# Kernel tuning notes

Hardware: AMD Instinct MI355X
Metric: run time of the kernel (lower is better)

The kernel has to match this reference:

```python
import jax, jax.numpy as jnp
import numpy as np

N = 50000   # num_entities
F = 300     # node feature dim
D = 128     # embedding_dim
H = 4       # heads
C = D // H  # per-head out channels (32)
E = 640000  # num edges
R = 200     # num_relations
L = 2       # num_layers
NEG_SLOPE = 0.2  # PyG GATv2Conv default


def setup_inputs() -> dict:
    key = jax.random.key(0)
    ks = jax.random.split(key, 14)
    s = 0.1
    return {
        "entity": jnp.arange(N, dtype=jnp.int32),
        "edge_index": jax.random.randint(ks[0], (2, E), 0, N, dtype=jnp.int32),
        "edge_type": jax.random.randint(ks[1], (E,), 0, R, dtype=jnp.int32),
        # learned parameters
        "node_features": jax.random.normal(ks[2], (N, F), jnp.float32) * s,   # entity_embedding table
        "rel_emb": jax.random.normal(ks[3], (R, D), jnp.float32) * s,          # relation_embedding
        "proj_w": jax.random.normal(ks[4], (F, D), jnp.float32) * s,           # project Linear
        "proj_b": jnp.zeros((D,), jnp.float32),
        # per-layer GATv2Conv params, stacked over L layers
        "w_l": jax.random.normal(ks[5], (L, D, H * C), jnp.float32) * s,       # lin_l weight
        "b_l": jnp.zeros((L, H * C), jnp.float32),
        "w_r": jax.random.normal(ks[6], (L, D, H * C), jnp.float32) * s,       # lin_r weight
        "b_r": jnp.zeros((L, H * C), jnp.float32),
        "w_e": jax.random.normal(ks[7], (L, D, H * C), jnp.float32) * s,       # lin_edge weight (no bias)
        "att": jax.random.normal(ks[8], (L, H, C), jnp.float32) * s,           # attention vector a
        "bias": jnp.zeros((L, H * C), jnp.float32),                             # output bias
    }


def _gatv2_layer(x, src, dst, edge_attr, w_l, b_l, w_r, b_r, w_e, att, bias):
    # x: [N, D], edge_attr: [E, D]
    x_l = (x @ w_l + b_l).reshape(N, H, C)
    x_r = (x @ w_r + b_r).reshape(N, H, C)
    e = (edge_attr @ w_e).reshape(E, H, C)
    # per-edge message (gather src/dst + edge), GATv2: leaky_relu BEFORE attention dot
    m = jax.nn.leaky_relu(x_l[src] + x_r[dst] + e, NEG_SLOPE)   # [E, H, C]
    logits = jnp.einsum('ehc,hc->eh', m, att)                    # [E, H]
    # segment softmax over edges grouped by destination node
    lmax = jax.ops.segment_max(logits, dst, num_segments=N)      # [N, H]
    ex = jnp.exp(logits - lmax[dst])                             # [E, H]
    denom = jax.ops.segment_sum(ex, dst, num_segments=N)         # [N, H]
    alpha = ex / denom[dst]                                      # [E, H]
    # scatter-aggregate messages x_l[src] weighted by alpha
    out = jax.ops.segment_sum(x_l[src] * alpha[:, :, None], dst, num_segments=N)  # [N, H, C]
    return out.reshape(N, H * C) + bias


def reference(entity, edge_index, edge_type, node_features, rel_emb,
              proj_w, proj_b, w_l, b_l, w_r, b_r, w_e, att, bias):
    x = node_features[entity]            # embedding lookup
    x = x @ proj_w + proj_b              # project to D
    edge_attr = rel_emb[edge_type]       # [E, D] (weights=False -> no edge_weight scaling)
    src, dst = edge_index[0], edge_index[1]
    for i in range(L):
        x = _gatv2_layer(x, src, dst, edge_attr,
                         w_l[i], b_l[i], w_r[i], b_r[i], w_e[i], att[i], bias[i])
        if i != L - 1:
            x = jax.nn.elu(x)            # dropout inactive (eval mode)
    return x
```

## Files before the change

kernel.cpp:

```cpp
#include <hip/hip_runtime.h>

#define NN 50000
#define FF 300
#define DD 128
#define HH 4
#define CC 32
#define EE 640000
#define RR 200
#define LL 2
#define SB ((NN + 255) / 256)
#define PK 320
#define WCONV (2 * 128 * 128)
#define WTOT (2 * 128 * PK + WCONV)
#define HB ((EE + 255) / 256)
#define WB (WCONV / 256)
#define FB PK
#define RB (LL * RR / 2)

typedef unsigned short u16;
typedef unsigned int u32;
typedef _Float16 h2   __attribute__((ext_vector_type(2)));
typedef _Float16 half8 __attribute__((ext_vector_type(8)));
typedef __attribute__((ext_vector_type(4))) float floatx4;

__device__ __forceinline__ u16 f2h(float f) {
    union { _Float16 h; u16 u; } v; v.h = (_Float16)f; return v.u;
}
__device__ __forceinline__ float h2f(u16 u) {
    union { u16 u; _Float16 h; } v; v.u = u; return (float)v.h;
}
__device__ __forceinline__ h2 u2h2(u32 p) {
    union { u32 u; h2 h; } v; v.u = p; return v.h;
}
__device__ __forceinline__ h2 hmax2(h2 a, h2 b) {
#if __has_builtin(__builtin_elementwise_max)
    return __builtin_elementwise_max(a, b);
#else
    h2 r; r.x = a.x > b.x ? a.x : b.x; r.y = a.y > b.y ? a.y : b.y; return r;
#endif
}
__device__ __forceinline__ float hdot2(h2 a, h2 b, float c) {
#if __has_builtin(__builtin_amdgcn_fdot2)
    return __builtin_amdgcn_fdot2(a, b, c, false);
#else
    return c + (float)a.x * (float)b.x + (float)a.y * (float)b.y;
#endif
}

__device__ __forceinline__ int block_excl_scan(int v, int* lds4, int* total) {
    int lane = threadIdx.x & 63, wid = threadIdx.x >> 6;
    int x = v;
    #pragma unroll
    for (int off = 1; off < 64; off <<= 1) {
        int y = __shfl_up(x, off, 64);
        if (lane >= off) x += y;
    }
    if (lane == 63) lds4[wid] = x;
    __syncthreads();
    int add = 0;
    #pragma unroll
    for (int w = 0; w < 4; w++) add += (w < wid) ? lds4[w] : 0;
    *total = lds4[0] + lds4[1] + lds4[2] + lds4[3];
    return x + add - v;
}

__global__ __launch_bounds__(256)
void prep_kernel(const int* __restrict__ ei, int* __restrict__ counts,
                 const float* __restrict__ proj_w, const float* __restrict__ w_l,
                 const float* __restrict__ w_r, u16* __restrict__ wt,
                 const float* __restrict__ rel_emb, const float* __restrict__ w_e,
                 u16* __restrict__ erel, const float* __restrict__ proj_b,
                 const float* __restrict__ b_l, const float* __restrict__ b_r,
                 float* __restrict__ fbias)
{
    __shared__ float rv[2][DD];
    int b = blockIdx.x, tid = threadIdx.x;
    if (b < HB) {
        int e = b * 256 + tid;
        if (e < EE) atomicAdd(&counts[ei[EE + e]], 1);
    } else if (b < HB + WB) {
        int i = (b - HB) * 256 + tid;
        int seg = i >> 14;
        int r = i & 16383;
        int n = r >> 7, k = r & 127;
        const float* src = (seg == 0 ? w_l : w_r) + (size_t)DD * DD;
        wt[2 * 128 * PK + i] = f2h(src[(size_t)k * DD + n]);
    } else if (b < HB + WB + FB) {
        int half = tid >> 7, d = tid & 127;
        int pp = (b - HB - WB) * 2 + half;
        int lr = pp / PK, k = pp - lr * PK;
        rv[half][d] = (k < FF) ? proj_w[(size_t)k * DD + d] : 0.f;
        __syncthreads();
        float acc = 0.f;
        if (k < FF) {
            const float* W = lr ? w_r : w_l;
            #pragma unroll 8
            for (int j = 0; j < DD; j++) acc += rv[half][j] * W[(size_t)j * DD + d];
        }
        wt[(size_t)lr * 128 * PK + (size_t)d * PK + k] = f2h(acc);
    } else if (b == HB + WB + FB) {
        int half = tid >> 7, d = tid & 127;
        if (tid < DD) rv[0][tid] = proj_b[tid];
        __syncthreads();
        const float* W = half ? w_r : w_l;
        float acc = half ? b_r[d] : b_l[d];
        #pragma unroll 8
        for (int j = 0; j < DD; j++) acc += rv[0][j] * W[(size_t)j * DD + d];
        fbias[half * DD + d] = acc;
    } else {
        int half = tid >> 7, d = tid & 127;
        int lr = (b - HB - WB - FB - 1) * 2 + half;
        int l = lr / RR, r = lr - l * RR;
        rv[half][d] = rel_emb[r * DD + d];
        __syncthreads();
        const float* W = w_e + (size_t)l * DD * DD;
        float acc = 0.f;
        #pragma unroll 8
        for (int k = 0; k < DD; k++) acc += rv[half][k] * W[k * DD + d];
        erel[(size_t)lr * DD + d] = f2h(acc);
    }
}

template<bool AF16, bool GATHER>
__global__ __launch_bounds__(256)
void gemm_dual_kernel(const void* __restrict__ A_, const int* __restrict__ rowidx,
                      int lda, int K, int Ka, int ldb,
                      const u16* __restrict__ BT1, const float* __restrict__ bias1,
                      u16* __restrict__ C1,
                      const u16* __restrict__ BT2, const float* __restrict__ bias2,
                      u16* __restrict__ C2, int M)
{
    __shared__ u16 As[64][72];
    __shared__ u16 Bs[256][72];
    int tid  = threadIdx.x;
    int m0   = blockIdx.x * 64;
    int wave = tid >> 6, lane = tid & 63;
    int quad = lane >> 4, l16 = lane & 15;
    int wcol = wave * 64;

    floatx4 acc[4][4];
    #pragma unroll
    for (int i = 0; i < 4; i++)
        #pragma unroll
        for (int j = 0; j < 4; j++) acc[i][j] = (floatx4){0.f, 0.f, 0.f, 0.f};

    int ar = tid >> 2, ak = (tid & 3) * 16;
    int arow = m0 + ar;
    int rid = (arow < M) ? (GATHER ? rowidx[arow] : arow) : 0;
    const u16* Brow = (tid < 128) ? (BT1 + (size_t)tid * ldb)
                                  : (BT2 + (size_t)(tid - 128) * ldb);

    for (int kk = 0; kk < K; kk += 64) {
        int kb = kk + ak;
        u16 tmp[16];
        if (AF16) {
            const u16* Ap = (const u16*)A_ + (size_t)rid * lda + kb;
            if (kb + 16 <= Ka) {
                *(half8*)&tmp[0] = *(const half8*)Ap;
                *(half8*)&tmp[8] = *(const half8*)(Ap + 8);
            } else {
                #pragma unroll
                for (int j = 0; j < 16; j++) tmp[j] = (kb + j < Ka) ? Ap[j] : (u16)0;
            }
        } else {
            const float* Ap = (const float*)A_ + (size_t)rid * lda + kb;
            if (kb + 16 <= Ka) {
                #pragma unroll
                for (int qq = 0; qq < 4; qq++) {
                    float4 f = *(const float4*)(Ap + qq * 4);
                    tmp[qq*4+0] = f2h(f.x); tmp[qq*4+1] = f2h(f.y);
                    tmp[qq*4+2] = f2h(f.z); tmp[qq*4+3] = f2h(f.w);
                }
            } else {
                #pragma unroll
                for (int j = 0; j < 16; j++) tmp[j] = (kb + j < Ka) ? f2h(Ap[j]) : (u16)0;
            }
        }
        *(half8*)&As[ar][ak]     = *(half8*)&tmp[0];
        *(half8*)&As[ar][ak + 8] = *(half8*)&tmp[8];
        #pragma unroll
        for (int q = 0; q < 8; q++)
            *(half8*)&Bs[tid][q * 8] = *(const half8*)(Brow + kk + q * 8);
        __syncthreads();
        #pragma unroll
        for (int ks = 0; ks < 2; ks++) {
            half8 af[4], bf[4];
            #pragma unroll
            for (int i = 0; i < 4; i++)
                af[i] = *(const half8*)&As[i * 16 + l16][ks * 32 + quad * 8];
            #pragma unroll
            for (int j = 0; j < 4; j++)
                bf[j] = *(const half8*)&Bs[wcol + j * 16 + l16][ks * 32 + quad * 8];
            #pragma unroll
            for (int i = 0; i < 4; i++)
                #pragma unroll
                for (int j = 0; j < 4; j++)
                    acc[i][j] = __builtin_amdgcn_mfma_f32_16x16x32_f16(
                        af[i], bf[j], acc[i][j], 0, 0, 0);
        }
        __syncthreads();
    }

    u16* Cw = (wave < 2) ? C1 : C2;
    const float* bw = (wave < 2) ? bias1 : bias2;
    int cbase = wcol & 127;
    #pragma unroll
    for (int i = 0; i < 4; i++) {
        #pragma unroll
        for (int rr = 0; rr < 4; rr++) {
            int row = m0 + i * 16 + quad * 4 + rr;
            if (row < M) {
                #pragma unroll
                for (int j = 0; j < 4; j++) {
                    int col = cbase + j * 16 + l16;
                    Cw[(size_t)row * DD + col] = f2h(acc[i][j][rr] + bw[col]);
                }
            }
        }
    }
}

__global__ __launch_bounds__(256)
void scan_local_kernel(const int* __restrict__ counts, int* __restrict__ offsets,
                       int* __restrict__ bsum)
{
    __shared__ int lds4[4];
    int i = blockIdx.x * 256 + threadIdx.x;
    int v = (i < NN) ? counts[i] : 0;
    int total;
    int ex = block_excl_scan(v, lds4, &total);
    if (i < NN) offsets[i] = ex;
    if (threadIdx.x == 0) bsum[blockIdx.x] = total;
}

__global__ __launch_bounds__(256)
void scan_bsum_kernel(int* __restrict__ bsum)
{
    __shared__ int lds4[4];
    int t = threadIdx.x;
    int v = (t < SB) ? bsum[t] : 0;
    int total;
    int ex = block_excl_scan(v, lds4, &total);
    if (t < SB) bsum[t] = ex;
}

__global__ __launch_bounds__(256)
void scatter_kernel(const int* __restrict__ ei, const int* __restrict__ et,
                    const int* __restrict__ offsets, const int* __restrict__ bsum,
                    int* __restrict__ fill, u32* __restrict__ dstorder)
{
    int e = blockIdx.x * 256 + threadIdx.x;
    if (e >= EE) return;
    int d = ei[EE + e];
    int pos = offsets[d] + bsum[d >> 8] + atomicAdd(&fill[d], 1);
    dstorder[pos] = (u32)ei[e] | ((u32)et[e] << 16);
}

__global__ __launch_bounds__(256)
void node_kernel(const u32* __restrict__ dstorder, const int* __restrict__ offsets,
                 const int* __restrict__ bsum,
                 const u16* __restrict__ xl, const u16* __restrict__ xr,
                 const u16* __restrict__ erel, const float* __restrict__ att,
                 const float* __restrict__ bias,
                 u16* __restrict__ xnext, float* __restrict__ outp, int is_last)
{
    int tid  = threadIdx.x;
    int node = blockIdx.x * 4 + (tid >> 6);
    int lane = tid & 63;
    if (node >= NN) return;
    int g  = lane >> 3;
    int gl = lane & 7;
    int c0 = gl * 16;
    int beg = offsets[node] + bsum[node >> 8];
    int end = (node == NN - 1) ? EE : offsets[node + 1] + bsum[(node + 1) >> 8];

    h2 xrh[8], atth[8];
    {
        const u32* xp = (const u32*)&xr[(size_t)node * DD + c0];
        #pragma unroll
        for (int q = 0; q < 8; q++) xrh[q] = u2h2(xp[q]);
        #pragma unroll
        for (int q = 0; q < 8; q++) {
            float2 av = *(const float2*)&att[c0 + q * 2];
            atth[q] = (h2){(_Float16)av.x, (_Float16)av.y};
        }
    }
    const h2 c02 = (h2){(_Float16)0.2f, (_Float16)0.2f};

    float s = 0.f;
    h2 a2[8];
    #pragma unroll
    for (int q = 0; q < 8; q++) a2[q] = (h2){(_Float16)0.f, (_Float16)0.f};

    int es = beg + g;
    u32 stB = (es + 8 < end) ? dstorder[es + 8] : 0u;
    h2 xhA[8], ehA[8];
    {
        u32 stA = (es < end) ? dstorder[es] : 0u;
        int src = stA & 0xffff, typ = stA >> 16;
        const u32* xp = (const u32*)&xl[(size_t)src * DD + c0];
        const u32* ep = (const u32*)&erel[(size_t)typ * DD + c0];
        #pragma unroll
        for (int q = 0; q < 8; q++) { xhA[q] = u2h2(xp[q]); ehA[q] = u2h2(ep[q]); }
    }

    for (int base = beg; base < end; base += 8) {
        u32 stN = (base + 16 + g < end) ? dstorder[base + 16 + g] : 0u;
        h2 xhB[8], ehB[8];
        {
            int src = stB & 0xffff, typ = stB >> 16;
            const u32* xp = (const u32*)&xl[(size_t)src * DD + c0];
            const u32* ep = (const u32*)&erel[(size_t)typ * DD + c0];
            #pragma unroll
            for (int q = 0; q < 8; q++) { xhB[q] = u2h2(xp[q]); ehB[q] = u2h2(ep[q]); }
        }
        float p = 0.f;
        #pragma unroll
        for (int q = 0; q < 8; q++) {
            h2 m = (xhA[q] + xrh[q]) + ehA[q];
            m = hmax2(m, m * c02);
            p = hdot2(m, atth[q], p);
        }
        p += __shfl_xor(p, 1, 64);
        bool valid = (base + g) < end;
        float w = valid ? __expf(fminf(p, 60.f)) : 0.f;
        s += w;
        h2 wh = (h2){(_Float16)w, (_Float16)w};
        #pragma unroll
        for (int q = 0; q < 8; q++) a2[q] += wh * xhA[q];
        #pragma unroll
        for (int q = 0; q < 8; q++) { xhA[q] = xhB[q]; ehA[q] = ehB[q]; }
        stB = stN;
    }

    float a[16];
    #pragma unroll
    for (int q = 0; q < 8; q++) { a[q*2] = (float)a2[q].x; a[q*2+1] = (float)a2[q].y; }
    #pragma unroll
    for (int j = 0; j < 16; j++) {
        a[j] += __shfl_xor(a[j], 8, 64);
        a[j] += __shfl_xor(a[j], 16, 64);
        a[j] += __shfl_xor(a[j], 32, 64);
    }
    s += __shfl_xor(s, 8, 64);
    s += __shfl_xor(s, 16, 64);
    s += __shfl_xor(s, 32, 64);

    if (lane < 8) {
        int cc = lane * 16;
        float rh = 1.f / fmaxf(s, 1e-30f);
        float bv[16], v[16];
        #pragma unroll
        for (int qq = 0; qq < 4; qq++) {
            float4 bq = *(const float4*)&bias[cc + qq * 4];
            bv[qq*4+0] = bq.x; bv[qq*4+1] = bq.y; bv[qq*4+2] = bq.z; bv[qq*4+3] = bq.w;
        }
        #pragma unroll
        for (int j = 0; j < 16; j++) v[j] = a[j] * rh + bv[j];
        if (is_last) {
            float4* op = (float4*)&outp[(size_t)node * DD + cc];
            #pragma unroll
            for (int qq = 0; qq < 4; qq++)
                op[qq] = make_float4(v[qq*4+0], v[qq*4+1], v[qq*4+2], v[qq*4+3]);
        } else {
            u16 pk[16];
            #pragma unroll
            for (int j = 0; j < 16; j++) {
                float w2 = v[j] > 0.f ? v[j] : __expf(v[j]) - 1.f;
                pk[j] = f2h(w2);
            }
            *(half8*)&xnext[(size_t)node * DD + cc]     = *(half8*)&pk[0];
            *(half8*)&xnext[(size_t)node * DD + cc + 8] = *(half8*)&pk[8];
        }
    }
}

extern "C" void kernel_launch(void* const* d_in, const int* in_sizes, int n_in,
                              void* d_out, int out_size, void* d_ws, size_t ws_size,
                              hipStream_t stream)
{
    const int*   entity        = (const int*)d_in[0];
    const int*   edge_index    = (const int*)d_in[1];
    const int*   edge_type     = (const int*)d_in[2];
    const float* node_features = (const float*)d_in[3];
    const float* rel_emb       = (const float*)d_in[4];
    const float* proj_w        = (const float*)d_in[5];
    const float* proj_b        = (const float*)d_in[6];
    const float* w_l           = (const float*)d_in[7];
    const float* b_l           = (const float*)d_in[8];
    const float* w_r           = (const float*)d_in[9];
    const float* b_r           = (const float*)d_in[10];
    const float* w_e           = (const float*)d_in[11];
    const float* att           = (const float*)d_in[12];
    const float* bias          = (const float*)d_in[13];

    u16*   xb      = (u16*)d_ws;
    u16*   xl      = xb + (size_t)NN * DD;
    u16*   xr      = xl + (size_t)NN * DD;
    u16*   erel    = xr + (size_t)NN * DD;
    u16*   wt      = erel + (size_t)LL * RR * DD;
    u32*   dstorder= (u32*)(wt + WTOT);
    int*   counts  = (int*)(dstorder + (size_t)EE);
    int*   fill    = counts + NN;
    int*   offsets = fill + NN;
    int*   bsum    = offsets + NN;
    float* fbias   = (float*)(bsum + SB);

    hipMemsetAsync(counts, 0, (size_t)NN * 2 * sizeof(int), stream);
    prep_kernel<<<HB + WB + FB + 1 + RB, 256, 0, stream>>>(
        edge_index, counts, proj_w, w_l, w_r, wt, rel_emb, w_e, erel,
        proj_b, b_l, b_r, fbias);

    scan_local_kernel<<<SB, 256, 0, stream>>>(counts, offsets, bsum);
    scan_bsum_kernel<<<1, 256, 0, stream>>>(bsum);
    scatter_kernel<<<(EE + 255) / 256, 256, 0, stream>>>(
        edge_index, edge_type, offsets, bsum, fill, dstorder);

    const int GB2 = (NN + 63) / 64;

    gemm_dual_kernel<false, true><<<GB2, 256, 0, stream>>>(
        node_features, entity, FF, PK, FF, PK,
        wt, fbias, xl,
        wt + (size_t)128 * PK, fbias + DD, xr, NN);
    node_kernel<<<(NN + 3) / 4, 256, 0, stream>>>(
        dstorder, offsets, bsum, xl, xr, erel,
        att, bias, xb, (float*)d_out, 0);

    gemm_dual_kernel<true, false><<<GB2, 256, 0, stream>>>(
        xb, nullptr, DD, DD, DD, DD,
        wt + (size_t)2 * 128 * PK, b_l + DD, xl,
        wt + (size_t)2 * 128 * PK + 128 * 128, b_r + DD, xr, NN);
    node_kernel<<<(NN + 3) / 4, 256, 0, stream>>>(
        dstorder, offsets, bsum, xl, xr, erel + (size_t)RR * DD,
        att + DD, bias + DD, xb, (float*)d_out, 1);
}
```

Measured before the change: 346.8 us.

## Read GEMM B operand directly from global and retile node kernel lanes

```diff
diff --git a/kernel.cpp b/kernel.cpp
--- a/kernel.cpp
+++ b/kernel.cpp
@@ -121,47 +121,45 @@
     }
 }
 
-template<bool AF16, bool GATHER>
-__global__ __launch_bounds__(256)
-void gemm_dual_kernel(const void* __restrict__ A_, const int* __restrict__ rowidx,
-                      int lda, int K, int Ka, int ldb,
-                      const u16* __restrict__ BT1, const float* __restrict__ bias1,
-                      u16* __restrict__ C1,
-                      const u16* __restrict__ BT2, const float* __restrict__ bias2,
-                      u16* __restrict__ C2, int M)
+template<bool AF16, bool GATHER, int K>
+__global__ __launch_bounds__(256)
+void gemm_bdirect_kernel(const void* __restrict__ A_, const int* __restrict__ rowidx,
+                         int lda, int Ka,
+                         const u16* __restrict__ BT1, const float* __restrict__ bias1,
+                         u16* __restrict__ C1,
+                         const u16* __restrict__ BT2, const float* __restrict__ bias2,
+                         u16* __restrict__ C2, int M)
 {
     __shared__ u16 As[64][72];
-    __shared__ u16 Bs[256][72];
     int tid  = threadIdx.x;
     int m0   = blockIdx.x * 64;
     int wave = tid >> 6, lane = tid & 63;
     int quad = lane >> 4, l16 = lane & 15;
-    int wcol = wave * 64;
+    const u16* BT = (wave < 2) ? BT1 : BT2;
+    int wcol = (wave & 1) * 64;
 
     floatx4 acc[4][4];
     #pragma unroll
     for (int i = 0; i < 4; i++)
         #pragma unroll
         for (int j = 0; j < 4; j++) acc[i][j] = (floatx4){0.f, 0.f, 0.f, 0.f};
+
+    const u16* Brow[4];
+    #pragma unroll
+    for (int j = 0; j < 4; j++) Brow[j] = BT + (size_t)(wcol + j * 16 + l16) * K;
 
     int ar = tid >> 2, ak = (tid & 3) * 16;
     int arow = m0 + ar;
     int rid = (arow < M) ? (GATHER ? rowidx[arow] : arow) : 0;
-    const u16* Brow = (tid < 128) ? (BT1 + (size_t)tid * ldb)
-                                  : (BT2 + (size_t)(tid - 128) * ldb);
-
+
+    #pragma unroll
     for (int kk = 0; kk < K; kk += 64) {
         int kb = kk + ak;
         u16 tmp[16];
         if (AF16) {
             const u16* Ap = (const u16*)A_ + (size_t)rid * lda + kb;
-            if (kb + 16 <= Ka) {
-                *(half8*)&tmp[0] = *(const half8*)Ap;
-                *(half8*)&tmp[8] = *(const half8*)(Ap + 8);
-            } else {
-                #pragma unroll
-                for (int j = 0; j < 16; j++) tmp[j] = (kb + j < Ka) ? Ap[j] : (u16)0;
-            }
+            *(half8*)&tmp[0] = *(const half8*)Ap;
+            *(half8*)&tmp[8] = *(const half8*)(Ap + 8);
         } else {
             const float* Ap = (const float*)A_ + (size_t)rid * lda + kb;
             if (kb + 16 <= Ka) {
@@ -178,9 +176,6 @@
         }
         *(half8*)&As[ar][ak]     = *(half8*)&tmp[0];
         *(half8*)&As[ar][ak + 8] = *(half8*)&tmp[8];
-        #pragma unroll
-        for (int q = 0; q < 8; q++)
-            *(half8*)&Bs[tid][q * 8] = *(const half8*)(Brow + kk + q * 8);
         __syncthreads();
         #pragma unroll
         for (int ks = 0; ks < 2; ks++) {
@@ -190,7 +185,7 @@
                 af[i] = *(const half8*)&As[i * 16 + l16][ks * 32 + quad * 8];
             #pragma unroll
             for (int j = 0; j < 4; j++)
-                bf[j] = *(const half8*)&Bs[wcol + j * 16 + l16][ks * 32 + quad * 8];
+                bf[j] = *(const half8*)(Brow[j] + kk + ks * 32 + quad * 8);
             #pragma unroll
             for (int i = 0; i < 4; i++)
                 #pragma unroll
@@ -203,7 +198,6 @@
 
     u16* Cw = (wave < 2) ? C1 : C2;
     const float* bw = (wave < 2) ? bias1 : bias2;
-    int cbase = wcol & 127;
     #pragma unroll
     for (int i = 0; i < 4; i++) {
         #pragma unroll
@@ -212,7 +206,7 @@
             if (row < M) {
                 #pragma unroll
                 for (int j = 0; j < 4; j++) {
-                    int col = cbase + j * 16 + l16;
+                    int col = wcol + j * 16 + l16;
                     Cw[(size_t)row * DD + col] = f2h(acc[i][j][rr] + bw[col]);
                 }
             }
@@ -268,19 +262,19 @@
     int node = blockIdx.x * 4 + (tid >> 6);
     int lane = tid & 63;
     if (node >= NN) return;
-    int g  = lane >> 3;
-    int gl = lane & 7;
-    int c0 = gl * 16;
+    int g  = lane >> 4;
+    int gl = lane & 15;
+    int c0 = gl * 8;
     int beg = offsets[node] + bsum[node >> 8];
     int end = (node == NN - 1) ? EE : offsets[node + 1] + bsum[(node + 1) >> 8];
 
-    h2 xrh[8], atth[8];
+    h2 xrh[4], atth[4];
     {
         const u32* xp = (const u32*)&xr[(size_t)node * DD + c0];
         #pragma unroll
-        for (int q = 0; q < 8; q++) xrh[q] = u2h2(xp[q]);
-        #pragma unroll
-        for (int q = 0; q < 8; q++) {
+        for (int q = 0; q < 4; q++) xrh[q] = u2h2(xp[q]);
+        #pragma unroll
+        for (int q = 0; q < 4; q++) {
             float2 av = *(const float2*)&att[c0 + q * 2];
             atth[q] = (h2){(_Float16)av.x, (_Float16)av.y};
         }
@@ -288,89 +282,67 @@
     const h2 c02 = (h2){(_Float16)0.2f, (_Float16)0.2f};
 
     float s = 0.f;
-    h2 a2[8];
-    #pragma unroll
-    for (int q = 0; q < 8; q++) a2[q] = (h2){(_Float16)0.f, (_Float16)0.f};
-
-    int es = beg + g;
-    u32 stB = (es + 8 < end) ? dstorder[es + 8] : 0u;
-    h2 xhA[8], ehA[8];
-    {
-        u32 stA = (es < end) ? dstorder[es] : 0u;
-        int src = stA & 0xffff, typ = stA >> 16;
+    h2 a2[4];
+    #pragma unroll
+    for (int q = 0; q < 4; q++) a2[q] = (h2){(_Float16)0.f, (_Float16)0.f};
+
+    for (int base = beg; base < end; base += 4) {
+        int es = base + g;
+        bool valid = es < end;
+        u32 st = valid ? dstorder[es] : 0;
+        int src = st & 0xffff;
+        int typ = st >> 16;
         const u32* xp = (const u32*)&xl[(size_t)src * DD + c0];
         const u32* ep = (const u32*)&erel[(size_t)typ * DD + c0];
-        #pragma unroll
-        for (int q = 0; q < 8; q++) { xhA[q] = u2h2(xp[q]); ehA[q] = u2h2(ep[q]); }
-    }
-
-    for (int base = beg; base < end; base += 8) {
-        u32 stN = (base + 16 + g < end) ? dstorder[base + 16 + g] : 0u;
-        h2 xhB[8], ehB[8];
-        {
-            int src = stB & 0xffff, typ = stB >> 16;
-            const u32* xp = (const u32*)&xl[(size_t)src * DD + c0];
-            const u32* ep = (const u32*)&erel[(size_t)typ * DD + c0];
-            #pragma unroll
-            for (int q = 0; q < 8; q++) { xhB[q] = u2h2(xp[q]); ehB[q] = u2h2(ep[q]); }
-        }
+        h2 xh[4];
         float p = 0.f;
         #pragma unroll
-        for (int q = 0; q < 8; q++) {
-            h2 m = (xhA[q] + xrh[q]) + ehA[q];
+        for (int q = 0; q < 4; q++) {
+            xh[q] = u2h2(xp[q]);
+            h2 m = (xh[q] + xrh[q]) + u2h2(ep[q]);
             m = hmax2(m, m * c02);
             p = hdot2(m, atth[q], p);
         }
         p += __shfl_xor(p, 1, 64);
-        bool valid = (base + g) < end;
+        p += __shfl_xor(p, 2, 64);
         float w = valid ? __expf(fminf(p, 60.f)) : 0.f;
         s += w;
         h2 wh = (h2){(_Float16)w, (_Float16)w};
         #pragma unroll
-        for (int q = 0; q < 8; q++) a2[q] += wh * xhA[q];
-        #pragma unroll
-        for (int q = 0; q < 8; q++) { xhA[q] = xhB[q]; ehA[q] = ehB[q]; }
-        stB = stN;
-    }
-
-    float a[16];
-    #pragma unroll
-    for (int q = 0; q < 8; q++) { a[q*2] = (float)a2[q].x; a[q*2+1] = (float)a2[q].y; }
-    #pragma unroll
-    for (int j = 0; j < 16; j++) {
-        a[j] += __shfl_xor(a[j], 8, 64);
+        for (int q = 0; q < 4; q++) a2[q] += wh * xh[q];
+    }
+
+    float a[8];
+    #pragma unroll
+    for (int q = 0; q < 4; q++) { a[q*2] = (float)a2[q].x; a[q*2+1] = (float)a2[q].y; }
+    #pragma unroll
+    for (int j = 0; j < 8; j++) {
         a[j] += __shfl_xor(a[j], 16, 64);
         a[j] += __shfl_xor(a[j], 32, 64);
     }
-    s += __shfl_xor(s, 8, 64);
     s += __shfl_xor(s, 16, 64);
     s += __shfl_xor(s, 32, 64);
 
-    if (lane < 8) {
-        int cc = lane * 16;
+    if (lane < 16) {
         float rh = 1.f / fmaxf(s, 1e-30f);
-        float bv[16], v[16];
-        #pragma unroll
-        for (int qq = 0; qq < 4; qq++) {
-            float4 bq = *(const float4*)&bias[cc + qq * 4];
-            bv[qq*4+0] = bq.x; bv[qq*4+1] = bq.y; bv[qq*4+2] = bq.z; bv[qq*4+3] = bq.w;
-        }
-        #pragma unroll
-        for (int j = 0; j < 16; j++) v[j] = a[j] * rh + bv[j];
+        float4 b0 = *(const float4*)&bias[c0];
+        float4 b1 = *(const float4*)&bias[c0 + 4];
+        float bv[8] = {b0.x, b0.y, b0.z, b0.w, b1.x, b1.y, b1.z, b1.w};
+        float v[8];
+        #pragma unroll
+        for (int j = 0; j < 8; j++) v[j] = a[j] * rh + bv[j];
         if (is_last) {
-            float4* op = (float4*)&outp[(size_t)node * DD + cc];
+            float4* op = (float4*)&outp[(size_t)node * DD + c0];
+            op[0] = make_float4(v[0], v[1], v[2], v[3]);
+            op[1] = make_float4(v[4], v[5], v[6], v[7]);
+        } else {
+            u16 pk[8];
             #pragma unroll
-            for (int qq = 0; qq < 4; qq++)
-                op[qq] = make_float4(v[qq*4+0], v[qq*4+1], v[qq*4+2], v[qq*4+3]);
-        } else {
-            u16 pk[16];
-            #pragma unroll
-            for (int j = 0; j < 16; j++) {
+            for (int j = 0; j < 8; j++) {
                 float w2 = v[j] > 0.f ? v[j] : __expf(v[j]) - 1.f;
                 pk[j] = f2h(w2);
             }
-            *(half8*)&xnext[(size_t)node * DD + cc]     = *(half8*)&pk[0];
-            *(half8*)&xnext[(size_t)node * DD + cc + 8] = *(half8*)&pk[8];
+            *(half8*)&xnext[(size_t)node * DD + c0] = *(half8*)pk;
         }
     }
 }
@@ -418,16 +390,16 @@
 
     const int GB2 = (NN + 63) / 64;
 
-    gemm_dual_kernel<false, true><<<GB2, 256, 0, stream>>>(
-        node_features, entity, FF, PK, FF, PK,
+    gemm_bdirect_kernel<false, true, PK><<<GB2, 256, 0, stream>>>(
+        node_features, entity, FF, FF,
         wt, fbias, xl,
         wt + (size_t)128 * PK, fbias + DD, xr, NN);
     node_kernel<<<(NN + 3) / 4, 256, 0, stream>>>(
         dstorder, offsets, bsum, xl, xr, erel,
         att, bias, xb, (float*)d_out, 0);
 
-    gemm_dual_kernel<true, false><<<GB2, 256, 0, stream>>>(
-        xb, nullptr, DD, DD, DD, DD,
+    gemm_bdirect_kernel<true, false, DD><<<GB2, 256, 0, stream>>>(
+        xb, nullptr, DD, DD,
         wt + (size_t)2 * 128 * PK, b_l + DD, xl,
         wt + (size_t)2 * 128 * PK + 128 * 128, b_r + DD, xr, NN);
     node_kernel<<<(NN + 3) / 4, 256, 0, stream>>>(
```

New measurement: 330.4 us. 1.05x faster.
